# Performance work log

Hardware: AMD Instinct MI355X
Metric: run time of the kernel (lower is better)

The kernel has to match this reference:

```python
import jax, jax.numpy as jnp
import numpy as np

FILTER_SIZE = 1024
NUM_HEADS = 16
D_HEAD = FILTER_SIZE // NUM_HEADS
LN_EPS = 1e-5


def setup_inputs() -> dict:
    key = jax.random.key(0)
    ks = jax.random.split(key, 10)
    B, T, D = 2, 2048, FILTER_SIZE
    s = 1.0 / np.sqrt(D)
    return {
        "x": jax.random.normal(ks[0], (B, T, D), dtype=jnp.float32),
        "Wq": jax.random.normal(ks[1], (D, D), dtype=jnp.float32) * s,
        "bq": jnp.zeros((D,), dtype=jnp.float32),
        "Wk": jax.random.normal(ks[2], (D, D), dtype=jnp.float32) * s,
        "bk": jnp.zeros((D,), dtype=jnp.float32),
        "Wv": jax.random.normal(ks[3], (D, D), dtype=jnp.float32) * s,
        "bv": jnp.zeros((D,), dtype=jnp.float32),
        "Wo": jax.random.normal(ks[4], (D, D), dtype=jnp.float32) * s,
        "bo": jnp.zeros((D,), dtype=jnp.float32),
        "gamma": jnp.ones((D,), dtype=jnp.float32),
        "beta": jnp.zeros((D,), dtype=jnp.float32),
    }


def reference(x, Wq, bq, Wk, bk, Wv, bv, Wo, bo, gamma, beta):
    B, T, D = x.shape
    H, Dh = NUM_HEADS, D_HEAD
    # Note: source splits features as (d_head, heads) with heads LAST.
    q = (x @ Wq.T + bq).reshape(B, T, Dh, H)
    k = (x @ Wk.T + bk).reshape(B, T, Dh, H)
    v = (x @ Wv.T + bv).reshape(B, T, Dh, H)
    scale = 1.0 / np.sqrt(Dh).astype(np.float32)
    # scores: (B, H, T, T)
    scores = jnp.einsum("bidh,bjdh->bhij", q, k) * scale
    attn = jax.nn.softmax(scores, axis=-1)  # dropout is identity in eval
    out = jnp.einsum("bhij,bjdh->bidh", attn, v)  # (B, T, Dh, H)
    out = out.reshape(B, T, D)  # matches permute(0,2,3,1).reshape in torch
    out = out @ Wo.T + bo
    out = out + x
    mu = jnp.mean(out, axis=-1, keepdims=True)
    var = jnp.var(out, axis=-1, keepdims=True)
    out = (out - mu) * jax.lax.rsqrt(var + LN_EPS) * gamma + beta
    return out
```

## Files before the change

### kernel.cpp

```cpp
#include <hip/hip_runtime.h>
#include <stdint.h>

#define T_SEQ 2048
#define D_MODEL 1024
#define NH 16
#define DH 64
#define NROWS 4096

typedef __bf16 bf16x8 __attribute__((ext_vector_type(8)));
typedef float floatx4 __attribute__((ext_vector_type(4)));
typedef short short4v __attribute__((ext_vector_type(4)));
typedef short short8v __attribute__((ext_vector_type(8)));

#define AS1 __attribute__((address_space(1)))
#define AS3 __attribute__((address_space(3)))

static __device__ __forceinline__ void gl2lds16(const unsigned short* g, unsigned short* s) {
    __builtin_amdgcn_global_load_lds((const AS1 unsigned int*)g, (AS3 unsigned int*)s, 16, 0, 0);
}

static __device__ __forceinline__ unsigned short f32_bf16(float f) {
    union { float f; unsigned int u; } c; c.f = f;
    unsigned int u = c.u;
    u = u + 0x7FFFu + ((u >> 16) & 1u);
    return (unsigned short)(u >> 16);
}

static __device__ __forceinline__ unsigned int pack2_bf16(float a, float b) {
    return (unsigned int)f32_bf16(a) | ((unsigned int)f32_bf16(b) << 16);
}

static __device__ __forceinline__ floatx4 mfma16(bf16x8 a, bf16x8 b, floatx4 c) {
    return __builtin_amdgcn_mfma_f32_16x16x32_bf16(a, b, c, 0, 0, 0);
}

static __device__ __forceinline__ bf16x8 as_bf(short8v s) {
    union { short8v s; bf16x8 b; } u; u.s = s; return u.b;
}

#define QSCALE 0.1803368801111204f
#define EXP2_SHIFT 10.0f
#define WAITCNT_VM(n) (0x0F70 | (n))

__global__ __launch_bounds__(256) void k_conv_all(const float* __restrict__ x,
                                                  const float* __restrict__ Wq,
                                                  const float* __restrict__ Wk,
                                                  const float* __restrict__ Wv,
                                                  const float* __restrict__ Wo,
                                                  unsigned short* __restrict__ x_bf,
                                                  unsigned short* __restrict__ wqkv_bf,
                                                  unsigned short* __restrict__ wo_bf) {
    int b = blockIdx.x, t = threadIdx.x;
    if (b < 4096) {
        int i = b * 1024 + t * 4;
        float4 v = *(const float4*)(x + i);
        uint2 o;
        o.x = pack2_bf16(v.x, v.y);
        o.y = pack2_bf16(v.z, v.w);
        *(uint2*)(x_bf + i) = o;
    } else if (b < 7168) {
        int idx = b - 4096;
        int tensor = idx >> 10, np = idx & 1023;
        const float* src = tensor == 0 ? Wq : tensor == 1 ? Wk : Wv;
        int f = (np & 63) * 16 + (np >> 6);
        int c = t * 4;
        float4 v = *(const float4*)(src + (long)f * D_MODEL + c);
        uint2 o;
        o.x = pack2_bf16(v.x, v.y);
        o.y = pack2_bf16(v.z, v.w);
        *(uint2*)(wqkv_bf + ((long)tensor * D_MODEL + np) * D_MODEL + c) = o;
    } else {
        int n = b - 7168;
        int fp = t * 4;
        const float* row = Wo + (long)n * D_MODEL;
        unsigned short o[4];
        #pragma unroll
        for (int k = 0; k < 4; k++) {
            int f = fp + k;
            o[k] = f32_bf16(row[(f & 63) * 16 + (f >> 6)]);
        }
        *(uint2*)(wo_bf + (long)n * D_MODEL + fp) = *(const uint2*)o;
    }
}

template <int BN, int MODE>
__global__ __launch_bounds__(256) void k_gemm(const unsigned short* __restrict__ A,
                                              const unsigned short* __restrict__ W,
                                              const float* __restrict__ b0,
                                              const float* __restrict__ b1,
                                              const float* __restrict__ b2,
                                              const float* __restrict__ resid,
                                              unsigned short* __restrict__ out_bf,
                                              unsigned short* __restrict__ vtg,
                                              float* __restrict__ out_f32) {
    constexpr int NT = BN / 32;
    constexpr int NCB = BN / 32;
    constexpr int NDMA = 4 + NCB;
    constexpr int NBUF = (MODE == 1) ? 2 : 1;
    __shared__ unsigned short lds_a[NBUF * 128 * 64];
    __shared__ unsigned short lds_b[NBUF * BN * 64];
    const int tid = threadIdx.x;
    const int w = tid >> 6, l = tid & 63;
    const int lrow = l & 15, lq = l >> 4;
    const int wm = (w >> 1) * 64, wn = (w & 1) * (BN / 2);
    const int L = blockIdx.x;
    const int bx = (L & 7) * 4 + ((L >> 3) & 3);
    const int by = L >> 5;
    const long am0 = (long)bx * 128;
    const long wn0 = (long)by * BN;

    floatx4 acc[4][NT] = {};
    const int grow = l >> 3;
    const int gcol = ((l & 7) ^ grow) * 8;
    const int sw8 = (lrow & 7);

    auto stage = [&](int ki, int sel) {
        unsigned short* la = lds_a + sel * 8192;
        unsigned short* lb = lds_b + sel * (BN * 64);
        int k0 = ki * 64;
        #pragma unroll
        for (int c = 0; c < 4; c++) {
            int chunk = w * 4 + c;
            gl2lds16(A + (am0 + chunk * 8 + grow) * D_MODEL + k0 + gcol, la + chunk * 512);
        }
        #pragma unroll
        for (int c = 0; c < NCB; c++) {
            int chunk = w * NCB + c;
            gl2lds16(W + (wn0 + chunk * 8 + grow) * D_MODEL + k0 + gcol, lb + chunk * 512);
        }
    };

    auto compute = [&](const unsigned short* la, const unsigned short* lb) {
        bf16x8 af[4][2], bfr[NT][2];
        #pragma unroll
        for (int mt = 0; mt < 4; mt++)
            #pragma unroll
            for (int ks = 0; ks < 2; ks++)
                af[mt][ks] = *(const bf16x8*)(la + (wm + mt * 16 + lrow) * 64 +
                                              (((ks * 4 + lq) ^ sw8) * 8));
        #pragma unroll
        for (int nt = 0; nt < NT; nt++)
            #pragma unroll
            for (int ks = 0; ks < 2; ks++)
                bfr[nt][ks] = *(const bf16x8*)(lb + (wn + nt * 16 + lrow) * 64 +
                                               (((ks * 4 + lq) ^ sw8) * 8));
        #pragma unroll
        for (int mt = 0; mt < 4; mt++)
            #pragma unroll
            for (int nt = 0; nt < NT; nt++)
                #pragma unroll
                for (int ks = 0; ks < 2; ks++)
                    acc[mt][nt] = mfma16(af[mt][ks], bfr[nt][ks], acc[mt][nt]);
    };

    if constexpr (MODE == 0) {
        for (int i = 0; i < 16; i++) {
            stage(i, 0);
            __builtin_amdgcn_s_waitcnt(WAITCNT_VM(0));
            __builtin_amdgcn_s_barrier();
            compute(lds_a, lds_b);
            __builtin_amdgcn_s_barrier();
        }
    } else {
        stage(0, 0);
        for (int i = 0; i < 16; i++) {
            const int cur = i & 1;
            if (i < 15) {
                stage(i + 1, 1 - cur);
                __builtin_amdgcn_s_waitcnt(WAITCNT_VM(NDMA));
            } else {
                __builtin_amdgcn_s_waitcnt(WAITCNT_VM(0));
            }
            __builtin_amdgcn_s_barrier();
            compute(lds_a + cur * 8192, lds_b + cur * (BN * 64));
            __builtin_amdgcn_s_barrier();
        }
    }

    if (MODE == 0) {
        int tensor = by >> 3;
        int nbase = (by & 7) * 128;
        const float* bias = tensor == 0 ? b0 : tensor == 1 ? b1 : b2;
        float scale = tensor == 0 ? QSCALE : 1.0f;
        if (tensor < 2) {
            unsigned short* outt = out_bf + (size_t)tensor * (32u * T_SEQ * DH);
            #pragma unroll
            for (int mt = 0; mt < 4; mt++) {
                #pragma unroll
                for (int nt = 0; nt < NT; nt++) {
                    int n = nbase + wn + nt * 16 + lrow;
                    int h = n >> 6, d = n & 63;
                    float bb = bias[d * 16 + h];
                    #pragma unroll
                    for (int r = 0; r < 4; r++) {
                        int row = (int)am0 + wm + mt * 16 + lq * 4 + r;
                        float v = (acc[mt][nt][r] + bb) * scale;
                        int b = row >> 11, i = row & 2047;
                        long idx = ((long)(b * 16 + h) * T_SEQ + i) * DH + d;
                        outt[idx] = f32_bf16(v);
                    }
                }
            }
        } else {
            int row0 = (int)am0 + wm;
            int b = row0 >> 11;
            int blk = (row0 & 2047) >> 6;
            #pragma unroll
            for (int nt = 0; nt < NT; nt++) {
                int n = nbase + wn + nt * 16 + lrow;
                int h = n >> 6, d = n & 63;
                float bb = bias[d * 16 + h];
                long base = (((long)(b * 16 + h) * 64 + d) * 32 + blk) * 64;
                #pragma unroll
                for (int mt = 0; mt < 4; mt++) {
                    uint2 o;
                    o.x = pack2_bf16(acc[mt][nt][0] + bb, acc[mt][nt][1] + bb);
                    o.y = pack2_bf16(acc[mt][nt][2] + bb, acc[mt][nt][3] + bb);
                    *(uint2*)(vtg + base + (mt >> 1) * 32 + lq * 8 + (mt & 1) * 4) = o;
                }
            }
        }
    } else {
        #pragma unroll
        for (int mt = 0; mt < 4; mt++) {
            #pragma unroll
            for (int nt = 0; nt < NT; nt++) {
                int n = (int)wn0 + wn + nt * 16 + lrow;
                float bb = b0[n];
                #pragma unroll
                for (int r = 0; r < 4; r++) {
                    int row = (int)am0 + wm + mt * 16 + lq * 4 + r;
                    long idx = (long)row * D_MODEL + n;
                    out_f32[idx] = acc[mt][nt][r] + bb + resid[idx];
                }
            }
        }
    }
}

__global__ __launch_bounds__(256) void k_attn(const unsigned short* __restrict__ q_ws,
                                              const unsigned short* __restrict__ k_ws,
                                              const unsigned short* __restrict__ vtg,
                                              unsigned short* __restrict__ att) {
    __shared__ unsigned short kbuf[2 * 64 * 64];
    __shared__ unsigned short vbuf[2 * 64 * 64];
    const int tid = threadIdx.x;
    const int w = tid >> 6, l = tid & 63;
    const int lrow = l & 15, lq = l >> 4;
    const int sw = lrow & 7;
    const int L = blockIdx.x;
    const int bh = (L & 7) * 4 + ((L >> 3) & 3);
    const int i0 = (L >> 5) * 128;
    const unsigned short* kh = k_ws + (long)bh * T_SEQ * DH;
    const unsigned short* vh = vtg + (long)bh * 64 * T_SEQ;

    const int rl = l >> 3;
    const int gl = ((l & 7) ^ rl) * 8;

    bf16x8 qf[2][2];
    #pragma unroll
    for (int qt = 0; qt < 2; qt++) {
        const unsigned short* qp =
            q_ws + ((long)bh * T_SEQ + i0 + w * 32 + qt * 16 + lrow) * DH + lq * 8;
        qf[qt][0] = *(const bf16x8*)qp;
        qf[qt][1] = *(const bf16x8*)(qp + 32);
    }
    floatx4 o_acc[2][4] = {};
    floatx4 l_acc[2] = {};
    const short8v ones8s = {0x3F80, 0x3F80, 0x3F80, 0x3F80, 0x3F80, 0x3F80, 0x3F80, 0x3F80};
    const bf16x8 ones8 = as_bf(ones8s);

    auto stage_k = [&](int jt, int sel) {
        unsigned short* kd = kbuf + sel * 4096 + (w * 2) * 512;
        #pragma unroll
        for (int c = 0; c < 2; c++) {
            int row = w * 16 + c * 8 + rl;
            gl2lds16(kh + ((long)(jt * 64 + row)) * 64 + gl, kd + c * 512);
        }
    };
    auto stage_v = [&](int jt, int sel) {
        unsigned short* vd = vbuf + sel * 4096 + (w * 2) * 512;
        #pragma unroll
        for (int c = 0; c < 2; c++) {
            int row = w * 16 + c * 8 + rl;
            gl2lds16(vh + ((long)row * 32 + jt) * 64 + gl, vd + c * 512);
        }
    };

    auto qk = [&](const unsigned short* kb_, floatx4 (&s0)[4], floatx4 (&s1)[4]) {
        #pragma unroll
        for (int nt = 0; nt < 4; nt++) {
            const unsigned short* kp = kb_ + (nt * 16 + lrow) * 64;
            bf16x8 ka = *(const bf16x8*)(kp + ((lq ^ sw) * 8));
            bf16x8 kb = *(const bf16x8*)(kp + (((lq + 4) ^ sw) * 8));
            floatx4 c0 = {-EXP2_SHIFT, -EXP2_SHIFT, -EXP2_SHIFT, -EXP2_SHIFT};
            floatx4 c1 = c0;
            c0 = mfma16(ka, qf[0][0], c0);
            c0 = mfma16(kb, qf[0][1], c0);
            c1 = mfma16(ka, qf[1][0], c1);
            c1 = mfma16(kb, qf[1][1], c1);
            s0[nt] = c0;
            s1[nt] = c1;
        }
    };

    auto sp4 = [&](floatx4 s) -> short4v {
        float p0 = __builtin_amdgcn_exp2f(s[0]);
        float p1 = __builtin_amdgcn_exp2f(s[1]);
        float p2 = __builtin_amdgcn_exp2f(s[2]);
        float p3 = __builtin_amdgcn_exp2f(s[3]);
        uint2 pk;
        pk.x = __builtin_amdgcn_perm(__float_as_uint(p1), __float_as_uint(p0), 0x07060302);
        pk.y = __builtin_amdgcn_perm(__float_as_uint(p3), __float_as_uint(p2), 0x07060302);
        union { uint2 u; short4v s4; } cv; cv.u = pk;
        return cv.s4;
    };

    auto pv_dt = [&](const unsigned short* vb_, int dt,
                     short8v (&p0)[2], short8v (&p1)[2]) {
        const unsigned short* vp = vb_ + (dt * 16 + lrow) * 64;
        bf16x8 vg0 = *(const bf16x8*)(vp + ((lq ^ sw) * 8));
        bf16x8 vg1 = *(const bf16x8*)(vp + (((4 + lq) ^ sw) * 8));
        o_acc[0][dt] = mfma16(vg0, as_bf(p0[0]), o_acc[0][dt]);
        o_acc[0][dt] = mfma16(vg1, as_bf(p0[1]), o_acc[0][dt]);
        o_acc[1][dt] = mfma16(vg0, as_bf(p1[0]), o_acc[1][dt]);
        o_acc[1][dt] = mfma16(vg1, as_bf(p1[1]), o_acc[1][dt]);
    };

    auto tile_body = [&](const unsigned short* kb_, const unsigned short* vb_,
                         short8v (&pp0)[2], short8v (&pp1)[2],
                         short8v (&pc0)[2], short8v (&pc1)[2]) {
        floatx4 s0[4], s1[4];
        qk(kb_, s0, s1);
        #pragma unroll
        for (int g = 0; g < 2; g++) {
            pv_dt(vb_, 2 * g, pp0, pp1);
            short4v t00 = sp4(s0[2 * g]);
            short4v t10 = sp4(s1[2 * g]);
            pv_dt(vb_, 2 * g + 1, pp0, pp1);
            short4v t01 = sp4(s0[2 * g + 1]);
            short4v t11 = sp4(s1[2 * g + 1]);
            pc0[g] = __builtin_shufflevector(t00, t01, 0, 1, 2, 3, 4, 5, 6, 7);
            pc1[g] = __builtin_shufflevector(t10, t11, 0, 1, 2, 3, 4, 5, 6, 7);
            l_acc[0] = mfma16(ones8, as_bf(pc0[g]), l_acc[0]);
            l_acc[1] = mfma16(ones8, as_bf(pc1[g]), l_acc[1]);
        }
    };

    short8v pA0[2], pA1[2], pB0[2], pB1[2];

    stage_k(0, 0);
    stage_k(1, 1);
    stage_v(0, 0);
    __builtin_amdgcn_s_waitcnt(WAITCNT_VM(4));
    __builtin_amdgcn_s_barrier();
    {
        floatx4 s0[4], s1[4];
        qk(kbuf, s0, s1);
        #pragma unroll
        for (int g = 0; g < 2; g++) {
            short4v t00 = sp4(s0[2 * g]);
            short4v t01 = sp4(s0[2 * g + 1]);
            short4v t10 = sp4(s1[2 * g]);
            short4v t11 = sp4(s1[2 * g + 1]);
            pA0[g] = __builtin_shufflevector(t00, t01, 0, 1, 2, 3, 4, 5, 6, 7);
            pA1[g] = __builtin_shufflevector(t10, t11, 0, 1, 2, 3, 4, 5, 6, 7);
            l_acc[0] = mfma16(ones8, as_bf(pA0[g]), l_acc[0]);
            l_acc[1] = mfma16(ones8, as_bf(pA1[g]), l_acc[1]);
        }
    }
    __builtin_amdgcn_s_barrier();

    for (int t = 1; t < 31; t += 2) {
        stage_k(t + 1, (t + 1) & 1);
        stage_v(t, t & 1);
        __builtin_amdgcn_s_waitcnt(WAITCNT_VM(4));
        __builtin_amdgcn_s_barrier();
        tile_body(kbuf + (t & 1) * 4096, vbuf + ((t - 1) & 1) * 4096,
                  pA0, pA1, pB0, pB1);
        __builtin_amdgcn_s_barrier();
        stage_k(t + 2, t & 1);
        stage_v(t + 1, (t + 1) & 1);
        __builtin_amdgcn_s_waitcnt(WAITCNT_VM(4));
        __builtin_amdgcn_s_barrier();
        tile_body(kbuf + ((t + 1) & 1) * 4096, vbuf + (t & 1) * 4096,
                  pB0, pB1, pA0, pA1);
        __builtin_amdgcn_s_barrier();
    }

    stage_v(31, 1);
    __builtin_amdgcn_s_waitcnt(WAITCNT_VM(2));
    __builtin_amdgcn_s_barrier();
    tile_body(kbuf + 4096, vbuf + 0, pA0, pA1, pB0, pB1);
    __builtin_amdgcn_s_barrier();

    __builtin_amdgcn_s_waitcnt(WAITCNT_VM(0));
    __builtin_amdgcn_s_barrier();
    #pragma unroll
    for (int dt = 0; dt < 4; dt++) pv_dt(vbuf + 4096, dt, pB0, pB1);

    int h = bh & 15, b = bh >> 4;
    #pragma unroll
    for (int qt = 0; qt < 2; qt++) {
        float rl2 = 1.0f / l_acc[qt][0];
        int i = i0 + w * 32 + qt * 16 + lrow;
        unsigned short* orow = att + ((long)(b * T_SEQ + i)) * D_MODEL + h * 64;
        #pragma unroll
        for (int dt = 0; dt < 4; dt++) {
            uint2 o;
            o.x = pack2_bf16(o_acc[qt][dt][0] * rl2, o_acc[qt][dt][1] * rl2);
            o.y = pack2_bf16(o_acc[qt][dt][2] * rl2, o_acc[qt][dt][3] * rl2);
            *(uint2*)(orow + dt * 16 + lq * 4) = o;
        }
    }
}

__global__ __launch_bounds__(256) void k_ln(float* __restrict__ io,
                                            const float* __restrict__ gamma,
                                            const float* __restrict__ beta) {
    int row = blockIdx.x, t = threadIdx.x;
    float* p = io + (long)row * D_MODEL + t * 4;
    float4 v = *(float4*)p;
    float s = v.x + v.y + v.z + v.w;
    float ss = v.x * v.x + v.y * v.y + v.z * v.z + v.w * v.w;
    #pragma unroll
    for (int m = 1; m < 64; m <<= 1) {
        s += __shfl_xor(s, m);
        ss += __shfl_xor(ss, m);
    }
    __shared__ float red[8];
    if ((t & 63) == 0) { red[t >> 6] = s; red[4 + (t >> 6)] = ss; }
    __syncthreads();
    s = red[0] + red[1] + red[2] + red[3];
    ss = red[4] + red[5] + red[6] + red[7];
    float mu = s * (1.0f / 1024.0f);
    float var = ss * (1.0f / 1024.0f) - mu * mu;
    float rstd = rsqrtf(var + 1e-5f);
    float4 g = *(const float4*)(gamma + t * 4);
    float4 be = *(const float4*)(beta + t * 4);
    float4 o;
    o.x = (v.x - mu) * rstd * g.x + be.x;
    o.y = (v.y - mu) * rstd * g.y + be.y;
    o.z = (v.z - mu) * rstd * g.z + be.z;
    o.w = (v.w - mu) * rstd * g.w + be.w;
    *(float4*)p = o;
}

extern "C" void kernel_launch(void* const* d_in, const int* in_sizes, int n_in,
                              void* d_out, int out_size, void* d_ws, size_t ws_size,
                              hipStream_t stream) {
    const float* x = (const float*)d_in[0];
    const float* Wq = (const float*)d_in[1];
    const float* bq = (const float*)d_in[2];
    const float* Wk = (const float*)d_in[3];
    const float* bk = (const float*)d_in[4];
    const float* Wv = (const float*)d_in[5];
    const float* bv = (const float*)d_in[6];
    const float* Wo = (const float*)d_in[7];
    const float* bo = (const float*)d_in[8];
    const float* gamma = (const float*)d_in[9];
    const float* beta = (const float*)d_in[10];
    float* out = (float*)d_out;

    char* ws = (char*)d_ws;
    unsigned short* x_bf = (unsigned short*)(ws);
    unsigned short* wqkv_bf = (unsigned short*)(ws + ((size_t)8 << 20));
    unsigned short* wo_bf = (unsigned short*)(ws + ((size_t)14 << 20));
    unsigned short* qkv_ws = (unsigned short*)(ws + ((size_t)16 << 20));
    unsigned short* att = x_bf;

    unsigned short* q_ws = qkv_ws;
    unsigned short* k_ws = qkv_ws + (size_t)32 * T_SEQ * DH;
    unsigned short* vtg = qkv_ws + (size_t)64 * T_SEQ * DH;

    k_conv_all<<<8192, 256, 0, stream>>>(x, Wq, Wk, Wv, Wo, x_bf, wqkv_bf, wo_bf);

    k_gemm<128, 0><<<768, 256, 0, stream>>>(
        x_bf, wqkv_bf, bq, bk, bv, nullptr, qkv_ws, vtg, nullptr);

    k_attn<<<512, 256, 0, stream>>>(q_ws, k_ws, vtg, att);

    k_gemm<64, 1><<<512, 256, 0, stream>>>(
        att, wo_bf, bo, nullptr, nullptr, x, nullptr, nullptr, out);

    k_ln<<<NROWS, 256, 0, stream>>>(out, gamma, beta);
}
```

Before: 216.6 us.

## Replace QKV projection GEMM with 256x256-tile double-buffered kernel

Adds a dedicated QKV projection kernel using 512 threads per block and 256x256 output tiles. It double-buffers K-slices in LDS, interleaving the next slice's global-to-LDS loads with MFMA work and raising wave priority around the MFMA bursts. The old 128x128 single-buffered GEMM path is removed and the output-projection GEMM is simplified to its double-buffered mode only. The larger tile raises data reuse and hides load latency, but only 192 blocks are launched and it uses 128 KB of LDS per block, which may leave some compute units idle.

```diff
diff --git a/kernel.cpp b/kernel.cpp
--- a/kernel.cpp
+++ b/kernel.cpp
@@ -83,22 +83,154 @@
     }
 }
 
+__global__ __launch_bounds__(512, 2) void k_qkv256(const unsigned short* __restrict__ A,
+                                                   const unsigned short* __restrict__ W,
+                                                   const float* __restrict__ bq,
+                                                   const float* __restrict__ bk,
+                                                   const float* __restrict__ bv,
+                                                   unsigned short* __restrict__ out_bf,
+                                                   unsigned short* __restrict__ vtg) {
+    __shared__ unsigned short lds[2 * 32768];
+    const int tid = threadIdx.x;
+    const int w = tid >> 6, l = tid & 63;
+    const int lrow = l & 15, lq = l >> 4;
+    const int sw8 = lrow & 7;
+    const int wm_id = w >> 2, wn_id = w & 3;
+    const int L = blockIdx.x;
+    const int bx = (L & 7) * 2 + ((L >> 3) & 1);
+    const int by = L >> 4;
+    const long am0 = (long)bx * 256;
+    const long wn0 = (long)by * 256;
+
+    const int rl = l >> 3;
+    const int gl = ((l & 7) ^ rl) * 8;
+
+    floatx4 acc[8][4] = {};
+
+    auto stage_piece = [&](int ki, int sel, int piece) {
+        int c = piece & 3;
+        int chunk = c * 8 + w;
+        int k0 = ki * 64;
+        if (piece < 4) {
+            gl2lds16(A + (am0 + chunk * 8 + rl) * D_MODEL + k0 + gl,
+                     lds + sel * 32768 + chunk * 512);
+        } else {
+            gl2lds16(W + (wn0 + chunk * 8 + rl) * D_MODEL + k0 + gl,
+                     lds + sel * 32768 + 16384 + chunk * 512);
+        }
+    };
+
+    #pragma unroll
+    for (int pc = 0; pc < 8; pc++) stage_piece(0, 0, pc);
+    __builtin_amdgcn_s_waitcnt(WAITCNT_VM(0));
+    __builtin_amdgcn_s_barrier();
+
+    for (int t = 0; t < 16; t++) {
+        const int sel = t & 1;
+        const unsigned short* Ab = lds + sel * 32768;
+        const unsigned short* Bb = Ab + 16384;
+        bf16x8 bfr[4];
+        #pragma unroll
+        for (int q = 0; q < 4; q++) {
+            const int ks = q >> 1, mh = q & 1;
+            if (mh == 0) {
+                #pragma unroll
+                for (int nt = 0; nt < 4; nt++) {
+                    int row = wn_id * 64 + nt * 16 + lrow;
+                    bfr[nt] = *(const bf16x8*)(Bb + row * 64 + (((ks * 4 + lq) ^ sw8) * 8));
+                }
+            }
+            bf16x8 af[4];
+            #pragma unroll
+            for (int j = 0; j < 4; j++) {
+                int row = wm_id * 128 + (mh * 4 + j) * 16 + lrow;
+                af[j] = *(const bf16x8*)(Ab + row * 64 + (((ks * 4 + lq) ^ sw8) * 8));
+            }
+            if (t < 15) {
+                if (q == 0) {
+                    stage_piece(t + 1, sel ^ 1, 0);
+                    stage_piece(t + 1, sel ^ 1, 1);
+                    stage_piece(t + 1, sel ^ 1, 2);
+                } else if (q == 1) {
+                    stage_piece(t + 1, sel ^ 1, 3);
+                    stage_piece(t + 1, sel ^ 1, 4);
+                    stage_piece(t + 1, sel ^ 1, 5);
+                } else if (q == 2) {
+                    stage_piece(t + 1, sel ^ 1, 6);
+                    stage_piece(t + 1, sel ^ 1, 7);
+                }
+            }
+            __builtin_amdgcn_s_barrier();
+            __builtin_amdgcn_s_setprio(1);
+            #pragma unroll
+            for (int j = 0; j < 4; j++)
+                #pragma unroll
+                for (int nt = 0; nt < 4; nt++)
+                    acc[mh * 4 + j][nt] = mfma16(af[j], bfr[nt], acc[mh * 4 + j][nt]);
+            __builtin_amdgcn_s_setprio(0);
+            if (q == 3 && t < 15)
+                __builtin_amdgcn_s_waitcnt(WAITCNT_VM(0));
+            __builtin_amdgcn_s_barrier();
+        }
+    }
+
+    int tensor = by >> 2;
+    int nbase = (by & 3) * 256;
+    const float* bias = tensor == 0 ? bq : tensor == 1 ? bk : bv;
+    float scale = tensor == 0 ? QSCALE : 1.0f;
+    if (tensor < 2) {
+        unsigned short* outt = out_bf + (size_t)tensor * (32u * T_SEQ * DH);
+        #pragma unroll
+        for (int mt = 0; mt < 8; mt++) {
+            #pragma unroll
+            for (int nt = 0; nt < 4; nt++) {
+                int n = nbase + wn_id * 64 + nt * 16 + lrow;
+                int h = n >> 6, d = n & 63;
+                float bb = bias[d * 16 + h];
+                #pragma unroll
+                for (int r = 0; r < 4; r++) {
+                    int row = (int)am0 + wm_id * 128 + mt * 16 + lq * 4 + r;
+                    float v = (acc[mt][nt][r] + bb) * scale;
+                    int b = row >> 11, i = row & 2047;
+                    long idx = ((long)(b * 16 + h) * T_SEQ + i) * DH + d;
+                    outt[idx] = f32_bf16(v);
+                }
+            }
+        }
+    } else {
+        int row0 = (int)am0 + wm_id * 128;
+        int b = row0 >> 11;
+        int blkb = (row0 & 2047) >> 6;
+        #pragma unroll
+        for (int nt = 0; nt < 4; nt++) {
+            int n = nbase + wn_id * 64 + nt * 16 + lrow;
+            int h = n >> 6, d = n & 63;
+            float bb = bias[d * 16 + h];
+            #pragma unroll
+            for (int mt = 0; mt < 8; mt++) {
+                int blk = blkb + (mt >> 2);
+                int m4 = mt & 3;
+                long base = (((long)(b * 16 + h) * 64 + d) * 32 + blk) * 64;
+                uint2 o;
+                o.x = pack2_bf16(acc[mt][nt][0] + bb, acc[mt][nt][1] + bb);
+                o.y = pack2_bf16(acc[mt][nt][2] + bb, acc[mt][nt][3] + bb);
+                *(uint2*)(vtg + base + (m4 >> 1) * 32 + lq * 8 + (m4 & 1) * 4) = o;
+            }
+        }
+    }
+}
+
 template <int BN, int MODE>
 __global__ __launch_bounds__(256) void k_gemm(const unsigned short* __restrict__ A,
                                               const unsigned short* __restrict__ W,
                                               const float* __restrict__ b0,
-                                              const float* __restrict__ b1,
-                                              const float* __restrict__ b2,
                                               const float* __restrict__ resid,
-                                              unsigned short* __restrict__ out_bf,
-                                              unsigned short* __restrict__ vtg,
                                               float* __restrict__ out_f32) {
     constexpr int NT = BN / 32;
     constexpr int NCB = BN / 32;
     constexpr int NDMA = 4 + NCB;
-    constexpr int NBUF = (MODE == 1) ? 2 : 1;
-    __shared__ unsigned short lds_a[NBUF * 128 * 64];
-    __shared__ unsigned short lds_b[NBUF * BN * 64];
+    __shared__ unsigned short lds_a[2 * 128 * 64];
+    __shared__ unsigned short lds_b[2 * BN * 64];
     const int tid = threadIdx.x;
     const int w = tid >> 6, l = tid & 63;
     const int lrow = l & 15, lq = l >> 4;
@@ -153,86 +285,31 @@
                     acc[mt][nt] = mfma16(af[mt][ks], bfr[nt][ks], acc[mt][nt]);
     };
 
-    if constexpr (MODE == 0) {
-        for (int i = 0; i < 16; i++) {
-            stage(i, 0);
+    stage(0, 0);
+    for (int i = 0; i < 16; i++) {
+        const int cur = i & 1;
+        if (i < 15) {
+            stage(i + 1, 1 - cur);
+            __builtin_amdgcn_s_waitcnt(WAITCNT_VM(NDMA));
+        } else {
             __builtin_amdgcn_s_waitcnt(WAITCNT_VM(0));
-            __builtin_amdgcn_s_barrier();
-            compute(lds_a, lds_b);
-            __builtin_amdgcn_s_barrier();
-        }
-    } else {
-        stage(0, 0);
-        for (int i = 0; i < 16; i++) {
-            const int cur = i & 1;
-            if (i < 15) {
-                stage(i + 1, 1 - cur);
-                __builtin_amdgcn_s_waitcnt(WAITCNT_VM(NDMA));
-            } else {
-                __builtin_amdgcn_s_waitcnt(WAITCNT_VM(0));
-            }
-            __builtin_amdgcn_s_barrier();
-            compute(lds_a + cur * 8192, lds_b + cur * (BN * 64));
-            __builtin_amdgcn_s_barrier();
-        }
-    }
-
-    if (MODE == 0) {
-        int tensor = by >> 3;
-        int nbase = (by & 7) * 128;
-        const float* bias = tensor == 0 ? b0 : tensor == 1 ? b1 : b2;
-        float scale = tensor == 0 ? QSCALE : 1.0f;
-        if (tensor < 2) {
-            unsigned short* outt = out_bf + (size_t)tensor * (32u * T_SEQ * DH);
-            #pragma unroll
-            for (int mt = 0; mt < 4; mt++) {
-                #pragma unroll
-                for (int nt = 0; nt < NT; nt++) {
-                    int n = nbase + wn + nt * 16 + lrow;
-                    int h = n >> 6, d = n & 63;
-                    float bb = bias[d * 16 + h];
-                    #pragma unroll
-                    for (int r = 0; r < 4; r++) {
-                        int row = (int)am0 + wm + mt * 16 + lq * 4 + r;
-                        float v = (acc[mt][nt][r] + bb) * scale;
-                        int b = row >> 11, i = row & 2047;
-                        long idx = ((long)(b * 16 + h) * T_SEQ + i) * DH + d;
-                        outt[idx] = f32_bf16(v);
-                    }
-                }
-            }
-        } else {
-            int row0 = (int)am0 + wm;
-            int b = row0 >> 11;
-            int blk = (row0 & 2047) >> 6;
-            #pragma unroll
-            for (int nt = 0; nt < NT; nt++) {
-                int n = nbase + wn + nt * 16 + lrow;
-                int h = n >> 6, d = n & 63;
-                float bb = bias[d * 16 + h];
-                long base = (((long)(b * 16 + h) * 64 + d) * 32 + blk) * 64;
-                #pragma unroll
-                for (int mt = 0; mt < 4; mt++) {
-                    uint2 o;
-                    o.x = pack2_bf16(acc[mt][nt][0] + bb, acc[mt][nt][1] + bb);
-                    o.y = pack2_bf16(acc[mt][nt][2] + bb, acc[mt][nt][3] + bb);
-                    *(uint2*)(vtg + base + (mt >> 1) * 32 + lq * 8 + (mt & 1) * 4) = o;
-                }
-            }
-        }
-    } else {
-        #pragma unroll
-        for (int mt = 0; mt < 4; mt++) {
-            #pragma unroll
-            for (int nt = 0; nt < NT; nt++) {
-                int n = (int)wn0 + wn + nt * 16 + lrow;
-                float bb = b0[n];
-                #pragma unroll
-                for (int r = 0; r < 4; r++) {
-                    int row = (int)am0 + wm + mt * 16 + lq * 4 + r;
-                    long idx = (long)row * D_MODEL + n;
-                    out_f32[idx] = acc[mt][nt][r] + bb + resid[idx];
-                }
+        }
+        __builtin_amdgcn_s_barrier();
+        compute(lds_a + cur * 8192, lds_b + cur * (BN * 64));
+        __builtin_amdgcn_s_barrier();
+    }
+
+    #pragma unroll
+    for (int mt = 0; mt < 4; mt++) {
+        #pragma unroll
+        for (int nt = 0; nt < NT; nt++) {
+            int n = (int)wn0 + wn + nt * 16 + lrow;
+            float bb = b0[n];
+            #pragma unroll
+            for (int r = 0; r < 4; r++) {
+                int row = (int)am0 + wm + mt * 16 + lq * 4 + r;
+                long idx = (long)row * D_MODEL + n;
+                out_f32[idx] = acc[mt][nt][r] + bb + resid[idx];
             }
         }
     }
@@ -475,13 +552,12 @@
 
     k_conv_all<<<8192, 256, 0, stream>>>(x, Wq, Wk, Wv, Wo, x_bf, wqkv_bf, wo_bf);
 
-    k_gemm<128, 0><<<768, 256, 0, stream>>>(
-        x_bf, wqkv_bf, bq, bk, bv, nullptr, qkv_ws, vtg, nullptr);
+    k_qkv256<<<192, 512, 0, stream>>>(x_bf, wqkv_bf, bq, bk, bv, qkv_ws, vtg);
 
     k_attn<<<512, 256, 0, stream>>>(q_ws, k_ws, vtg, att);
 
     k_gemm<64, 1><<<512, 256, 0, stream>>>(
-        att, wo_bf, bo, nullptr, nullptr, x, nullptr, nullptr, out);
+        att, wo_bf, bo, x, out);
 
     k_ln<<<NROWS, 256, 0, stream>>>(out, gamma, beta);
 }
```

After: 195.7 us. -9.6%, faster.
